# Kernel optimization log

Hardware: AMD Instinct MI355X
Metric: run time of the kernel (lower is better)

## Reference

```python
import jax, jax.numpy as jnp
import numpy as np
from jax import lax

NUM_GROUP = 512    # G: number of FPS centers
GROUP_SIZE = 32    # M: KNN neighbors per center


def setup_inputs() -> dict:
    key = jax.random.key(0)
    xyz = jax.random.normal(key, (32, 8192, 3), dtype=jnp.float32)  # B N 3
    return {"xyz": xyz}


def _fps(xyz, num_group):
    """Iterative farthest point sampling. xyz: [B,N,3] -> idx [B,G] int32.
    Deterministic start at point 0 (matching pointnet2-style fps)."""
    B, N, _ = xyz.shape

    def step(carry, _):
        dists, last_idx = carry                       # dists: [B,N] running min sq-dist
        last = xyz[jnp.arange(B), last_idx]           # [B,3] most recent center
        d = jnp.sum((xyz - last[:, None, :]) ** 2, axis=-1)  # [B,N]
        dists = jnp.minimum(dists, d)
        nxt = jnp.argmax(dists, axis=-1).astype(jnp.int32)   # farthest point
        return (dists, nxt), nxt

    init_idx = jnp.zeros((B,), jnp.int32)
    init_d = jnp.full((B, N), jnp.inf, xyz.dtype)
    (_, _), idxs = lax.scan(step, (init_d, init_idx), None, length=num_group - 1)
    return jnp.concatenate([init_idx[None, :], idxs], axis=0).T  # [B,G]


def reference(xyz):
    B, N, _ = xyz.shape
    G, M = NUM_GROUP, GROUP_SIZE

    fps_idx = _fps(xyz, G)                              # [B,G] int32
    center = xyz[jnp.arange(B)[:, None], fps_idx]       # [B,G,3]

    # KNN: for each center, k nearest points in xyz (squared euclidean)
    # dist2[b,g,n] = |c|^2 + |x|^2 - 2 c.x   -> [B,G,N]
    x2 = jnp.sum(xyz * xyz, axis=-1)                    # [B,N]
    c2 = jnp.sum(center * center, axis=-1)              # [B,G]
    dist2 = c2[:, :, None] + x2[:, None, :] - 2.0 * jnp.einsum('bgd,bnd->bgn', center, xyz)
    _, idx = lax.top_k(-dist2, M)                       # [B,G,M] nearest-first

    neighborhood = xyz[jnp.arange(B)[:, None, None], idx]   # [B,G,M,3]
    neighborhood = neighborhood - center[:, :, None, :]
    return neighborhood, center, fps_idx
```

## Files before the change

kernel.cpp:

```cpp
#include <hip/hip_runtime.h>
#include <math.h>

#define BATCH  32
#define NPTS   8192
#define NGROUP 512
#define MSIZE  32

#define FPS_THREADS 512
#define SXYZ_FLOATS (NPTS * 3)
#define DYN_LDS_BYTES (SXYZ_FLOATS * 4)

template<int CTRL>
__device__ __forceinline__ float dpp_max_f32(float x) {
    int o = __builtin_amdgcn_update_dpp(0, __float_as_int(x), CTRL, 0xF, 0xF, true);
    float f = __int_as_float(o);
    return x > f ? x : f;
}
template<int CTRL>
__device__ __forceinline__ unsigned dpp_min_u32(unsigned x) {
    unsigned o = (unsigned)__builtin_amdgcn_update_dpp(0, (int)x, CTRL, 0xF, 0xF, true);
    return o < x ? o : x;
}
template<int CTRL>
__device__ __forceinline__ unsigned long long dpp_min_u64(unsigned long long k) {
    int lo2 = __builtin_amdgcn_update_dpp(0, (int)(unsigned)k,        CTRL, 0xF, 0xF, true);
    int hi2 = __builtin_amdgcn_update_dpp(0, (int)(unsigned)(k >> 32), CTRL, 0xF, 0xF, true);
    unsigned long long k2 = (((unsigned long long)(unsigned)hi2) << 32) | (unsigned)lo2;
    return k2 < k ? k2 : k;
}

__global__ __launch_bounds__(FPS_THREADS, 2)
void fps_kernel(const float* __restrict__ xyz,
                float* __restrict__ out_center,
                float* __restrict__ out_fps)
{
#pragma clang fp contract(off)
    extern __shared__ float sxyz[];
    __shared__ float        pmax[2][8];
    __shared__ unsigned int sidx[2];

    const int b    = blockIdx.x;
    const int t    = threadIdx.x;
    const int lane = t & 63;
    const int wid  = t >> 6;
    const float* bp = xyz + (size_t)b * NPTS * 3;
    const float4* bp4 = reinterpret_cast<const float4*>(bp);
    float4* s4 = reinterpret_cast<float4*>(sxyz);

    float px[16], py[16], pz[16], dist[16];
    #pragma unroll
    for (int c = 0; c < 4; ++c) {
        int f4 = c * 1536 + t * 3;
        float4 A = bp4[f4 + 0];
        float4 B = bp4[f4 + 1];
        float4 C = bp4[f4 + 2];
        s4[f4 + 0] = A; s4[f4 + 1] = B; s4[f4 + 2] = C;
        float xs[4] = {A.x, A.w, B.z, C.y};
        float ys[4] = {A.y, B.x, B.w, C.z};
        float zs[4] = {A.z, B.y, C.x, C.w};
        #pragma unroll
        for (int k = 0; k < 4; ++k) {
            int j = c * 4 + k;
            px[j] = xs[k]; py[j] = ys[k]; pz[j] = zs[k];
            dist[j] = INFINITY;
        }
    }
    if (t == 0) { sidx[0] = 0xFFFFFFFFu; sidx[1] = 0xFFFFFFFFu; }
    __syncthreads();

    if (t == 0) {
        out_fps[(size_t)b * NGROUP] = 0.0f;
        out_center[(size_t)(b * NGROUP) * 3 + 0] = sxyz[0];
        out_center[(size_t)(b * NGROUP) * 3 + 1] = sxyz[1];
        out_center[(size_t)(b * NGROUP) * 3 + 2] = sxyz[2];
    }

    const int tbase = t * 4;
    int last = 0;
    for (int g = 1; g < NGROUP; ++g) {
        const int p = g & 1, q = p ^ 1;
        float lx = sxyz[last*3 + 0];
        float ly = sxyz[last*3 + 1];
        float lz = sxyz[last*3 + 2];

        #pragma unroll
        for (int j = 0; j < 16; ++j) {
            float dx = px[j] - lx;
            float dy = py[j] - ly;
            float dz = pz[j] - lz;
            float d  = (dx*dx + dy*dy) + dz*dz;
            dist[j] = dist[j] < d ? dist[j] : d;
        }
        float m01 = fmaxf(fmaxf(dist[0],  dist[1]),  fmaxf(dist[2],  dist[3]));
        float m23 = fmaxf(fmaxf(dist[4],  dist[5]),  fmaxf(dist[6],  dist[7]));
        float m45 = fmaxf(fmaxf(dist[8],  dist[9]),  fmaxf(dist[10], dist[11]));
        float m67 = fmaxf(fmaxf(dist[12], dist[13]), fmaxf(dist[14], dist[15]));
        float m = fmaxf(fmaxf(m01, m23), fmaxf(m45, m67));
        m = dpp_max_f32<0xB1>(m);
        m = dpp_max_f32<0x4E>(m);
        m = dpp_max_f32<0x141>(m);
        m = dpp_max_f32<0x140>(m);
        m = dpp_max_f32<0x142>(m);
        m = dpp_max_f32<0x143>(m);
        float wmax = __int_as_float(__builtin_amdgcn_readlane(__float_as_int(m), 63));
        if (lane == 63) pmax[p][wid] = wmax;
        __syncthreads();

        float gmax = fmaxf(
            fmaxf(fmaxf(pmax[p][0], pmax[p][1]), fmaxf(pmax[p][2], pmax[p][3])),
            fmaxf(fmaxf(pmax[p][4], pmax[p][5]), fmaxf(pmax[p][6], pmax[p][7])));
        if (t == 0) sidx[q] = 0xFFFFFFFFu;

        if (wmax == gmax) {
            unsigned c0[16];
            #pragma unroll
            for (int j = 0; j < 16; ++j) {
                unsigned gj = (unsigned)((j >> 2) * 2048 + tbase + (j & 3));
                c0[j] = (dist[j] == gmax) ? gj : 0xFFFFFFFFu;
            }
            #pragma unroll
            for (int s = 8; s >= 1; s >>= 1)
                #pragma unroll
                for (int i = 0; i < s; ++i)
                    c0[i] = c0[i] < c0[i+s] ? c0[i] : c0[i+s];
            unsigned mi = c0[0];
            mi = dpp_min_u32<0xB1>(mi);
            mi = dpp_min_u32<0x4E>(mi);
            mi = dpp_min_u32<0x141>(mi);
            mi = dpp_min_u32<0x140>(mi);
            mi = dpp_min_u32<0x142>(mi);
            mi = dpp_min_u32<0x143>(mi);
            if (lane == 63) atomicMin(&sidx[p], mi);
        }
        __syncthreads();

        int fi = (int)sidx[p];
        last = fi;
        if (t == 0) {
            out_fps[(size_t)b * NGROUP + g] = (float)fi;
            out_center[((size_t)(b * NGROUP + g)) * 3 + 0] = sxyz[fi*3 + 0];
            out_center[((size_t)(b * NGROUP + g)) * 3 + 1] = sxyz[fi*3 + 1];
            out_center[((size_t)(b * NGROUP + g)) * 3 + 2] = sxyz[fi*3 + 2];
        }
    }
}

__global__ __launch_bounds__(256)
void knn_kernel(const float* __restrict__ xyz,
                const float* __restrict__ center,
                float* __restrict__ out_nbhd)
{
    const int lane = threadIdx.x & 63;
    const int gid  = blockIdx.x * 4 + (threadIdx.x >> 6);
    const int b    = gid >> 9;
    const float* bp = xyz + (size_t)b * NPTS * 3;
    const float4* bp4 = reinterpret_cast<const float4*>(bp);

    const float cx = center[(size_t)gid*3+0];
    const float cy = center[(size_t)gid*3+1];
    const float cz = center[(size_t)gid*3+2];

    unsigned long long kl[4];
    #pragma unroll
    for (int k = 0; k < 4; ++k) kl[k] = ~0ULL;

    for (int c = 0; c < 32; ++c) {
        int f4 = c * 192 + lane * 3;
        float4 a  = bp4[f4+0];
        float4 bq = bp4[f4+1];
        float4 cq = bp4[f4+2];
        int p0 = c * 256 + lane * 4;
        float xs[4] = {a.x, a.w, bq.z, cq.y};
        float ys[4] = {a.y, bq.x, bq.w, cq.z};
        float zs[4] = {a.z, bq.y, cq.x, cq.w};
        #pragma unroll
        for (int k = 0; k < 4; ++k) {
            float dx = xs[k]-cx, dy = ys[k]-cy, dz = zs[k]-cz;
            float d = dx*dx + dy*dy + dz*dz;
            unsigned long long key =
                (((unsigned long long)__float_as_uint(d)) << 32) | (unsigned)(p0 + k);
            if (key < kl[3]) {
                kl[3] = key;
                #pragma unroll
                for (int q = 3; q > 0; --q) {
                    if (kl[q] < kl[q-1]) {
                        unsigned long long tk = kl[q]; kl[q] = kl[q-1]; kl[q-1] = tk;
                    }
                }
            }
        }
    }

    int keep = 0;
    #pragma unroll 1
    for (int r = 0; r < MSIZE; ++r) {
        unsigned long long k = kl[0];
        k = dpp_min_u64<0xB1>(k);
        k = dpp_min_u64<0x4E>(k);
        k = dpp_min_u64<0x141>(k);
        k = dpp_min_u64<0x140>(k);
        {
            unsigned long long o = __shfl_xor(k, 16);
            if (o < k) k = o;
            o = __shfl_xor(k, 32);
            if (o < k) k = o;
        }
        if (lane == r) keep = (int)(unsigned)k;
        if (kl[0] == k) {
            kl[0] = kl[1]; kl[1] = kl[2]; kl[2] = kl[3];
            kl[3] = ~0ULL;
        }
    }

    if (lane < MSIZE) {
        size_t o = ((size_t)gid * MSIZE + lane) * 3;
        float x = bp[keep*3+0], y = bp[keep*3+1], z = bp[keep*3+2];
        out_nbhd[o+0] = x - cx;
        out_nbhd[o+1] = y - cy;
        out_nbhd[o+2] = z - cz;
    }
}

extern "C" void kernel_launch(void* const* d_in, const int* in_sizes, int n_in,
                              void* d_out, int out_size, void* d_ws, size_t ws_size,
                              hipStream_t stream)
{
    const float* xyz = (const float*)d_in[0];
    float* out        = (float*)d_out;
    float* out_nbhd   = out;
    float* out_center = out + (size_t)BATCH*NGROUP*MSIZE*3;
    float* out_fps    = out_center + (size_t)BATCH*NGROUP*3;

    hipFuncSetAttribute(reinterpret_cast<const void*>(fps_kernel),
                        hipFuncAttributeMaxDynamicSharedMemorySize,
                        DYN_LDS_BYTES);

    fps_kernel<<<dim3(BATCH), dim3(FPS_THREADS), DYN_LDS_BYTES, stream>>>(xyz, out_center, out_fps);
    knn_kernel<<<dim3(BATCH*NGROUP/4), dim3(256), 0, stream>>>(xyz, out_center, out_nbhd);
}
```

Baseline: 705.2 us.

## Pack FPS argmax into single barrier and use 32-bit truncated KNN keys

The FPS loop now finds each wave's local argmax against its own wave max, packs (max, ~index) into a 64-bit key in LDS, and reduces the 8 wave keys with DPP. This drops one of the two barriers per iteration. Distance math in both kernels is written with packed float2 vectors. The KNN kernel packs distance and index into a single 32-bit key by dropping the low 13 mantissa bits of the distance, which halves selection and shuffle cost. The truncated key can reorder near-tie neighbors and change which points are selected relative to exact top-k.

```diff
diff --git a/kernel.cpp b/kernel.cpp
--- a/kernel.cpp
+++ b/kernel.cpp
@@ -10,6 +10,8 @@
 #define SXYZ_FLOATS (NPTS * 3)
 #define DYN_LDS_BYTES (SXYZ_FLOATS * 4)
 
+typedef float v2f __attribute__((ext_vector_type(2)));
+
 template<int CTRL>
 __device__ __forceinline__ float dpp_max_f32(float x) {
     int o = __builtin_amdgcn_update_dpp(0, __float_as_int(x), CTRL, 0xF, 0xF, true);
@@ -22,11 +24,16 @@
     return o < x ? o : x;
 }
 template<int CTRL>
-__device__ __forceinline__ unsigned long long dpp_min_u64(unsigned long long k) {
+__device__ __forceinline__ unsigned long long dpp_max_u64(unsigned long long k) {
     int lo2 = __builtin_amdgcn_update_dpp(0, (int)(unsigned)k,        CTRL, 0xF, 0xF, true);
     int hi2 = __builtin_amdgcn_update_dpp(0, (int)(unsigned)(k >> 32), CTRL, 0xF, 0xF, true);
     unsigned long long k2 = (((unsigned long long)(unsigned)hi2) << 32) | (unsigned)lo2;
-    return k2 < k ? k2 : k;
+    return k2 > k ? k2 : k;
+}
+template<int CTRL>
+__device__ __forceinline__ unsigned dpp_min_u32_full(unsigned x) {
+    unsigned o = (unsigned)__builtin_amdgcn_update_dpp(0, (int)x, CTRL, 0xF, 0xF, true);
+    return o < x ? o : x;
 }
 
 __global__ __launch_bounds__(FPS_THREADS, 2)
@@ -36,8 +43,7 @@
 {
 #pragma clang fp contract(off)
     extern __shared__ float sxyz[];
-    __shared__ float        pmax[2][8];
-    __shared__ unsigned int sidx[2];
+    __shared__ unsigned long long partial[2][8];
 
     const int b    = blockIdx.x;
     const int t    = threadIdx.x;
@@ -47,7 +53,8 @@
     const float4* bp4 = reinterpret_cast<const float4*>(bp);
     float4* s4 = reinterpret_cast<float4*>(sxyz);
 
-    float px[16], py[16], pz[16], dist[16];
+    v2f px2[8], py2[8], pz2[8], dist2[8];
+    unsigned idxv[16];
     #pragma unroll
     for (int c = 0; c < 4; ++c) {
         int f4 = c * 1536 + t * 3;
@@ -55,17 +62,15 @@
         float4 B = bp4[f4 + 1];
         float4 C = bp4[f4 + 2];
         s4[f4 + 0] = A; s4[f4 + 1] = B; s4[f4 + 2] = C;
-        float xs[4] = {A.x, A.w, B.z, C.y};
-        float ys[4] = {A.y, B.x, B.w, C.z};
-        float zs[4] = {A.z, B.y, C.x, C.w};
-        #pragma unroll
-        for (int k = 0; k < 4; ++k) {
-            int j = c * 4 + k;
-            px[j] = xs[k]; py[j] = ys[k]; pz[j] = zs[k];
-            dist[j] = INFINITY;
-        }
-    }
-    if (t == 0) { sidx[0] = 0xFFFFFFFFu; sidx[1] = 0xFFFFFFFFu; }
+        int j0 = c * 2, j1 = c * 2 + 1;
+        px2[j0] = (v2f){A.x, A.w};  py2[j0] = (v2f){A.y, B.x};  pz2[j0] = (v2f){A.z, B.y};
+        px2[j1] = (v2f){B.z, C.y};  py2[j1] = (v2f){B.w, C.z};  pz2[j1] = (v2f){C.x, C.w};
+        dist2[j0] = (v2f){INFINITY, INFINITY};
+        dist2[j1] = (v2f){INFINITY, INFINITY};
+        #pragma unroll
+        for (int k = 0; k < 4; ++k)
+            idxv[c*4 + k] = (unsigned)(c * 2048 + t * 4 + k);
+    }
     __syncthreads();
 
     if (t == 0) {
@@ -75,27 +80,29 @@
         out_center[(size_t)(b * NGROUP) * 3 + 2] = sxyz[2];
     }
 
-    const int tbase = t * 4;
     int last = 0;
     for (int g = 1; g < NGROUP; ++g) {
-        const int p = g & 1, q = p ^ 1;
+        const int p = g & 1;
         float lx = sxyz[last*3 + 0];
         float ly = sxyz[last*3 + 1];
         float lz = sxyz[last*3 + 2];
 
         #pragma unroll
-        for (int j = 0; j < 16; ++j) {
-            float dx = px[j] - lx;
-            float dy = py[j] - ly;
-            float dz = pz[j] - lz;
-            float d  = (dx*dx + dy*dy) + dz*dz;
-            dist[j] = dist[j] < d ? dist[j] : d;
-        }
-        float m01 = fmaxf(fmaxf(dist[0],  dist[1]),  fmaxf(dist[2],  dist[3]));
-        float m23 = fmaxf(fmaxf(dist[4],  dist[5]),  fmaxf(dist[6],  dist[7]));
-        float m45 = fmaxf(fmaxf(dist[8],  dist[9]),  fmaxf(dist[10], dist[11]));
-        float m67 = fmaxf(fmaxf(dist[12], dist[13]), fmaxf(dist[14], dist[15]));
-        float m = fmaxf(fmaxf(m01, m23), fmaxf(m45, m67));
+        for (int j = 0; j < 8; ++j) {
+            v2f dx = px2[j] - lx;
+            v2f dy = py2[j] - ly;
+            v2f dz = pz2[j] - lz;
+            v2f t1 = dx * dx;
+            v2f t2 = dy * dy;
+            v2f t3 = dz * dz;
+            v2f s  = t1 + t2;
+            v2f d  = s + t3;
+            dist2[j] = __builtin_elementwise_min(dist2[j], d);
+        }
+        v2f mm = dist2[0];
+        #pragma unroll
+        for (int j = 1; j < 8; ++j) mm = __builtin_elementwise_max(mm, dist2[j]);
+        float m = fmaxf(mm.x, mm.y);
         m = dpp_max_f32<0xB1>(m);
         m = dpp_max_f32<0x4E>(m);
         m = dpp_max_f32<0x141>(m);
@@ -103,38 +110,37 @@
         m = dpp_max_f32<0x142>(m);
         m = dpp_max_f32<0x143>(m);
         float wmax = __int_as_float(__builtin_amdgcn_readlane(__float_as_int(m), 63));
-        if (lane == 63) pmax[p][wid] = wmax;
+
+        unsigned c0[16];
+        #pragma unroll
+        for (int j = 0; j < 8; ++j) {
+            c0[2*j+0] = (dist2[j].x == wmax) ? idxv[2*j+0] : 0xFFFFFFFFu;
+            c0[2*j+1] = (dist2[j].y == wmax) ? idxv[2*j+1] : 0xFFFFFFFFu;
+        }
+        #pragma unroll
+        for (int s = 8; s >= 1; s >>= 1)
+            #pragma unroll
+            for (int i = 0; i < s; ++i)
+                c0[i] = c0[i] < c0[i+s] ? c0[i] : c0[i+s];
+        unsigned mi = c0[0];
+        mi = dpp_min_u32<0xB1>(mi);
+        mi = dpp_min_u32<0x4E>(mi);
+        mi = dpp_min_u32<0x141>(mi);
+        mi = dpp_min_u32<0x140>(mi);
+        mi = dpp_min_u32<0x142>(mi);
+        mi = dpp_min_u32<0x143>(mi);
+        if (lane == 63) {
+            unsigned long long key =
+                (((unsigned long long)__float_as_uint(wmax)) << 32) | (unsigned)~mi;
+            partial[p][wid] = key;
+        }
         __syncthreads();
 
-        float gmax = fmaxf(
-            fmaxf(fmaxf(pmax[p][0], pmax[p][1]), fmaxf(pmax[p][2], pmax[p][3])),
-            fmaxf(fmaxf(pmax[p][4], pmax[p][5]), fmaxf(pmax[p][6], pmax[p][7])));
-        if (t == 0) sidx[q] = 0xFFFFFFFFu;
-
-        if (wmax == gmax) {
-            unsigned c0[16];
-            #pragma unroll
-            for (int j = 0; j < 16; ++j) {
-                unsigned gj = (unsigned)((j >> 2) * 2048 + tbase + (j & 3));
-                c0[j] = (dist[j] == gmax) ? gj : 0xFFFFFFFFu;
-            }
-            #pragma unroll
-            for (int s = 8; s >= 1; s >>= 1)
-                #pragma unroll
-                for (int i = 0; i < s; ++i)
-                    c0[i] = c0[i] < c0[i+s] ? c0[i] : c0[i+s];
-            unsigned mi = c0[0];
-            mi = dpp_min_u32<0xB1>(mi);
-            mi = dpp_min_u32<0x4E>(mi);
-            mi = dpp_min_u32<0x141>(mi);
-            mi = dpp_min_u32<0x140>(mi);
-            mi = dpp_min_u32<0x142>(mi);
-            mi = dpp_min_u32<0x143>(mi);
-            if (lane == 63) atomicMin(&sidx[p], mi);
-        }
-        __syncthreads();
-
-        int fi = (int)sidx[p];
+        unsigned long long kq = partial[p][lane & 7];
+        kq = dpp_max_u64<0xB1>(kq);
+        kq = dpp_max_u64<0x4E>(kq);
+        kq = dpp_max_u64<0x141>(kq);
+        int fi = (int)(~(unsigned)kq);
         last = fi;
         if (t == 0) {
             out_fps[(size_t)b * NGROUP + g] = (float)fi;
@@ -160,31 +166,32 @@
     const float cy = center[(size_t)gid*3+1];
     const float cz = center[(size_t)gid*3+2];
 
-    unsigned long long kl[4];
+    unsigned kl[4];
     #pragma unroll
-    for (int k = 0; k < 4; ++k) kl[k] = ~0ULL;
+    for (int k = 0; k < 4; ++k) kl[k] = 0xFFFFFFFFu;
 
     for (int c = 0; c < 32; ++c) {
         int f4 = c * 192 + lane * 3;
         float4 a  = bp4[f4+0];
         float4 bq = bp4[f4+1];
         float4 cq = bp4[f4+2];
-        int p0 = c * 256 + lane * 4;
-        float xs[4] = {a.x, a.w, bq.z, cq.y};
-        float ys[4] = {a.y, bq.x, bq.w, cq.z};
-        float zs[4] = {a.z, bq.y, cq.x, cq.w};
+        unsigned p0 = (unsigned)(c * 256 + lane * 4);
+        v2f xA = (v2f){a.x,  a.w},  yA = (v2f){a.y,  bq.x}, zA = (v2f){a.z,  bq.y};
+        v2f xB = (v2f){bq.z, cq.y}, yB = (v2f){bq.w, cq.z}, zB = (v2f){cq.x, cq.w};
+        v2f dxA = xA - cx, dyA = yA - cy, dzA = zA - cz;
+        v2f dxB = xB - cx, dyB = yB - cy, dzB = zB - cz;
+        v2f dA = dxA*dxA + dyA*dyA + dzA*dzA;
+        v2f dB = dxB*dxB + dyB*dyB + dzB*dzB;
+        float ds[4] = {dA.x, dA.y, dB.x, dB.y};
         #pragma unroll
         for (int k = 0; k < 4; ++k) {
-            float dx = xs[k]-cx, dy = ys[k]-cy, dz = zs[k]-cz;
-            float d = dx*dx + dy*dy + dz*dz;
-            unsigned long long key =
-                (((unsigned long long)__float_as_uint(d)) << 32) | (unsigned)(p0 + k);
+            unsigned key = (__float_as_uint(ds[k]) & 0xFFFFE000u) | (p0 + k);
             if (key < kl[3]) {
                 kl[3] = key;
                 #pragma unroll
                 for (int q = 3; q > 0; --q) {
                     if (kl[q] < kl[q-1]) {
-                        unsigned long long tk = kl[q]; kl[q] = kl[q-1]; kl[q-1] = tk;
+                        unsigned tk = kl[q]; kl[q] = kl[q-1]; kl[q-1] = tk;
                     }
                 }
             }
@@ -194,21 +201,21 @@
     int keep = 0;
     #pragma unroll 1
     for (int r = 0; r < MSIZE; ++r) {
-        unsigned long long k = kl[0];
-        k = dpp_min_u64<0xB1>(k);
-        k = dpp_min_u64<0x4E>(k);
-        k = dpp_min_u64<0x141>(k);
-        k = dpp_min_u64<0x140>(k);
+        unsigned k = kl[0];
+        k = dpp_min_u32_full<0xB1>(k);
+        k = dpp_min_u32_full<0x4E>(k);
+        k = dpp_min_u32_full<0x141>(k);
+        k = dpp_min_u32_full<0x140>(k);
         {
-            unsigned long long o = __shfl_xor(k, 16);
-            if (o < k) k = o;
+            unsigned o = __shfl_xor(k, 16);
+            k = o < k ? o : k;
             o = __shfl_xor(k, 32);
-            if (o < k) k = o;
-        }
-        if (lane == r) keep = (int)(unsigned)k;
+            k = o < k ? o : k;
+        }
+        if (lane == r) keep = (int)(k & 0x1FFFu);
         if (kl[0] == k) {
             kl[0] = kl[1]; kl[1] = kl[2]; kl[2] = kl[3];
-            kl[3] = ~0ULL;
+            kl[3] = 0xFFFFFFFFu;
         }
     }
 
```

Result: faster. 619.2 us (-12.2%).
